# Kernel tuning notes

Hardware: AMD Instinct MI355X
Metric: run time of the kernel (lower is better)

The kernel has to match this reference:

```python
import jax, jax.numpy as jnp
import numpy as np

N_NODES = 50000
IN_DIM = 128
OUT_DIM = 128
HEADS = 4
HEAD_DIM = OUT_DIM // HEADS
N_EDGES = 800000
LN_EPS = 1e-5
NEG_SLOPE = 0.2


def setup_inputs() -> dict:
    key = jax.random.key(0)
    ks = jax.random.split(key, 8)
    x = jax.random.normal(ks[0], (N_NODES, IN_DIM), dtype=jnp.float32)
    edge_index = jax.random.randint(ks[1], (2, N_EDGES), 0, N_NODES, dtype=jnp.int64)
    s = 1.0 / np.sqrt(IN_DIM)
    W = jax.random.uniform(ks[2], (IN_DIM, HEADS * HEAD_DIM), jnp.float32, -s, s)
    att_src = jax.random.uniform(ks[3], (HEADS, HEAD_DIM), jnp.float32, -s, s)
    att_dst = jax.random.uniform(ks[4], (HEADS, HEAD_DIM), jnp.float32, -s, s)
    bias = jnp.zeros((OUT_DIM,), jnp.float32)
    gamma = jnp.ones((OUT_DIM,), jnp.float32)
    beta = jnp.zeros((OUT_DIM,), jnp.float32)
    return {"x": x, "edge_index": edge_index, "W": W, "att_src": att_src,
            "att_dst": att_dst, "bias": bias, "gamma": gamma, "beta": beta}


def reference(x, edge_index, W, att_src, att_dst, bias, gamma, beta):
    N = x.shape[0]
    H, C = att_src.shape
    # add self-loops (PyG GATConv default)
    loops = jnp.arange(N, dtype=edge_index.dtype)
    src = jnp.concatenate([edge_index[0], loops])  # [E+N]
    dst = jnp.concatenate([edge_index[1], loops])

    h = (x @ W).reshape(N, H, C)                      # [N,H,C]
    a_src = jnp.einsum('nhc,hc->nh', h, att_src)      # [N,H]
    a_dst = jnp.einsum('nhc,hc->nh', h, att_dst)

    e = jax.nn.leaky_relu(a_src[src] + a_dst[dst], NEG_SLOPE)   # [E+N,H]
    emax = jax.ops.segment_max(e, dst, num_segments=N)          # [N,H]
    ex = jnp.exp(e - emax[dst])
    denom = jax.ops.segment_sum(ex, dst, num_segments=N)
    alpha = ex / denom[dst]                                     # [E+N,H]

    msg = h[src] * alpha[:, :, None]                            # [E+N,H,C]
    out = jax.ops.segment_sum(msg, dst, num_segments=N).reshape(N, H * C) + bias

    # LayerNorm
    mu = out.mean(-1, keepdims=True)
    var = ((out - mu) ** 2).mean(-1, keepdims=True)
    hn = (out - mu) / jnp.sqrt(var + LN_EPS) * gamma + beta

    # residual is Identity (in_dim == out_dim); GELU exact; dropout = eval identity
    return jax.nn.gelu(hn + x, approximate=False)
```

## Files before the change

kernel.cpp:

```cpp
#include <hip/hip_runtime.h>
#include <math.h>

#define N_NODES 50000
#define HEADS 4
#define NEG_SLOPE 0.2f
#define LN_EPS 1e-5f
#define SLOTS 80
#define GR 64
#define EPB 2048
#define DSH 8
#define NB 196
#define CAP 40

typedef short short8 __attribute__((ext_vector_type(8)));
typedef float f32x4 __attribute__((ext_vector_type(4)));


__device__ __forceinline__ short f2bf(float f) {
    unsigned u = __float_as_uint(f);
    return (short)((u + 0x7fffu + ((u >> 16) & 1u)) >> 16);
}

__device__ __forceinline__ void load_edge(const int* __restrict__ ei, int e, int E,
                                          int is64, int& s, int& d) {
    if (is64) {
        s = ei[2 * e];
        d = ei[2 * (E + e)];
    } else {
        s = ei[e];
        d = ei[E + e];
    }
}

__device__ __forceinline__ int detect_is64(const int* __restrict__ ei, int t, int* s_flag) {
    if (t < 64) {
        int nz = (ei[2 * t + 1] != 0) ? 1 : 0;
        unsigned long long b = __ballot(nz);
        if (t == 0) *s_flag = (b == 0ULL) ? 1 : 0;
    }
    __syncthreads();
    return *s_flag;
}

__device__ __forceinline__ float s8f(unsigned u, int p) {
    return (float)((int)(u << (24 - 8 * p)) >> 24);
}

__device__ __forceinline__ float edge_w(float v) {
    v = v > 0.f ? v : NEG_SLOPE * v;
    return __expf(v);
}


__global__ __launch_bounds__(256, 4) void gemm_scatter_kernel(
    const float* __restrict__ x, const float* __restrict__ W,
    const float* __restrict__ att_src, const float* __restrict__ att_dst,
    unsigned* __restrict__ hb, float* __restrict__ hscale,
    float* __restrict__ a_src, float* __restrict__ a_dst,
    const int* __restrict__ ei, int E, int nScatter, int nGemm,
    unsigned* __restrict__ staging, int* __restrict__ scnt) {
    __shared__ __align__(16) char smem[40960];
    const int t = threadIdx.x;
    const int b = (int)blockIdx.x;

    const bool isBin = (b % 3) == 0;
    const int rid = isBin ? (b / 3) : (2 * (b / 3) + (b % 3) - 1);

    if (isBin) {
        if (rid >= nScatter) return;
        int is64 = detect_is64(ei, t, (int*)smem);
        int* lcnt = (int*)smem + 64;
        for (int i = t; i < NB; i += 256) lcnt[i] = 0;
        __syncthreads();

        const int e0 = rid * EPB + t;
        int ss[8], dd[8];
#pragma unroll
        for (int u = 0; u < 8; ++u) {
            int e = e0 + u * 256;
            if (e < E) {
                load_edge(ei, e, E, is64, ss[u], dd[u]);
            } else {
                ss[u] = -1; dd[u] = 0;
            }
        }
#pragma unroll
        for (int u = 0; u < 8; ++u) {
            if (ss[u] < 0) continue;
            int bkt = dd[u] >> DSH;
            int p = atomicAdd(&lcnt[bkt], 1);
            if (p < CAP)
                staging[((size_t)bkt * nScatter + rid) * CAP + p] =
                    (unsigned)ss[u] | ((unsigned)dd[u] << 16);
        }
        __syncthreads();
        for (int i = t; i < NB; i += 256)
            scnt[(size_t)i * nScatter + rid] = min(lcnt[i], CAP);
        return;
    }

    if (rid >= nGemm) return;
    const int rowBase = rid * GR;
    const int l = t & 63;
    const int wv = t >> 6;

    {
        const int nlo = l & 7, khi = l >> 3;
        for (int i = 0; i < 8; ++i) {
            int tile = wv + 4 * i;
            int n = (tile & 15) * 8 + nlo;
            int k8 = (tile >> 4) * 8 + khi;
            short8 pk;
#pragma unroll
            for (int jj = 0; jj < 8; ++jj)
                pk[jj] = f2bf(W[(k8 * 8 + jj) * 128 + n]);
            int us = (k8 & 8) | ((k8 & 7) ^ (n & 7));
            *(short8*)(smem + n * 256 + us * 16) = pk;
        }
    }
    __syncthreads();

    const int g = l >> 4;
    const int c = l & 15;

    f32x4 acc[8];
#pragma unroll
    for (int ct = 0; ct < 8; ++ct) acc[ct] = {0.f, 0.f, 0.f, 0.f};

    {
        int arow = rowBase + wv * 16 + c;
        if (arow >= N_NODES) arow = N_NODES - 1;
        const float* xrow = x + (size_t)arow * 128;
#pragma unroll
        for (int kk = 0; kk < 4; ++kk) {
            float4 xa = *(const float4*)(xrow + kk * 32 + g * 8);
            float4 xb = *(const float4*)(xrow + kk * 32 + g * 8 + 4);
            short8 af;
            af[0] = f2bf(xa.x); af[1] = f2bf(xa.y); af[2] = f2bf(xa.z); af[3] = f2bf(xa.w);
            af[4] = f2bf(xb.x); af[5] = f2bf(xb.y); af[6] = f2bf(xb.z); af[7] = f2bf(xb.w);
#pragma unroll
            for (int ct = 0; ct < 8; ++ct) {
                int n = ct * 16 + c;
                int u = kk * 4 + g;
                int us = (u & 8) | ((u & 7) ^ (n & 7));
                short8 bf = *(const short8*)(smem + n * 256 + us * 16);
                acc[ct] = __builtin_amdgcn_mfma_f32_16x16x32_bf16(af, bf, acc[ct], 0, 0, 0);
            }
        }
    }

    char* ep = smem + 32768 + wv * 2048;
    float asA[4], asB[4], adA[4], adB[4];
#pragma unroll
    for (int h = 0; h < 4; ++h) {
        asA[h] = att_src[h * 32 + c];
        asB[h] = att_src[h * 32 + 16 + c];
        adA[h] = att_dst[h * 32 + c];
        adB[h] = att_dst[h * 32 + 16 + c];
    }
#pragma unroll
    for (int r = 0; r < 4; ++r) {
        float v[8];
#pragma unroll
        for (int ct = 0; ct < 8; ++ct) v[ct] = acc[ct][r];

        float m = fabsf(v[0]);
#pragma unroll
        for (int ct = 1; ct < 8; ++ct) m = fmaxf(m, fabsf(v[ct]));
#pragma unroll
        for (int o = 1; o < 16; o <<= 1) m = fmaxf(m, __shfl_xor(m, o, 64));
        m = fmaxf(m, 1e-20f);
        const float inv = 127.0f / m;

        float sp[4], dp[4];
#pragma unroll
        for (int h = 0; h < 4; ++h) {
            sp[h] = v[2 * h] * asA[h] + v[2 * h + 1] * asB[h];
            dp[h] = v[2 * h] * adA[h] + v[2 * h + 1] * adB[h];
        }
#pragma unroll
        for (int o = 1; o < 16; o <<= 1) {
#pragma unroll
            for (int h = 0; h < 4; ++h) {
                sp[h] += __shfl_xor(sp[h], o, 64);
                dp[h] += __shfl_xor(dp[h], o, 64);
            }
        }
        const int row_l = g * 4 + r;
        const int row = rowBase + wv * 16 + row_l;
        if (c == 0 && row < N_NODES) {
            hscale[row] = m * (1.0f / 127.0f);
            a_src[row * 4 + 0] = sp[0]; a_src[row * 4 + 1] = sp[1];
            a_src[row * 4 + 2] = sp[2]; a_src[row * 4 + 3] = sp[3];
            a_dst[row * 4 + 0] = dp[0]; a_dst[row * 4 + 1] = dp[1];
            a_dst[row * 4 + 2] = dp[2]; a_dst[row * 4 + 3] = dp[3];
        }
#pragma unroll
        for (int ct = 0; ct < 8; ++ct) {
            int q = __float2int_rn(v[ct] * inv);
            ep[row_l * 128 + ct * 16 + c] = (char)q;
        }
    }

#pragma unroll
    for (int w8 = 0; w8 < 8; ++w8) {
        int idx = w8 * 64 + l;
        int row_l = idx >> 5, tx = idx & 31;
        unsigned word = *(const unsigned*)(ep + row_l * 128 + tx * 4);
        int row = rowBase + wv * 16 + row_l;
        if (row < N_NODES) hb[(size_t)row * 32 + tx] = word;
    }
}

__global__ __launch_bounds__(256) void build_kernel(
    const unsigned* __restrict__ staging, const int* __restrict__ scnt,
    int nScatter, int* __restrict__ cnt, unsigned short* __restrict__ esrc) {
    __shared__ int lcnt2[256];
    const int B = blockIdx.x;
    const int t = threadIdx.x;
    lcnt2[t] = 0;
    __syncthreads();

    for (int blk = t; blk < nScatter; blk += 256) {
        const int c = scnt[(size_t)B * nScatter + blk];
        const unsigned* cell = staging + ((size_t)B * nScatter + blk) * CAP;
        for (int j = 0; j < c; j += 4) {
            uint4 q = *(const uint4*)(cell + j);
            const int m = c - j;
            {
                int d = (int)(q.x >> 16);
                int p = atomicAdd(&lcnt2[d & 255], 1);
                if (p < SLOTS) esrc[(size_t)d * SLOTS + p] = (unsigned short)(q.x & 0xffffu);
            }
            if (m > 1) {
                int d = (int)(q.y >> 16);
                int p = atomicAdd(&lcnt2[d & 255], 1);
                if (p < SLOTS) esrc[(size_t)d * SLOTS + p] = (unsigned short)(q.y & 0xffffu);
            }
            if (m > 2) {
                int d = (int)(q.z >> 16);
                int p = atomicAdd(&lcnt2[d & 255], 1);
                if (p < SLOTS) esrc[(size_t)d * SLOTS + p] = (unsigned short)(q.z & 0xffffu);
            }
            if (m > 3) {
                int d = (int)(q.w >> 16);
                int p = atomicAdd(&lcnt2[d & 255], 1);
                if (p < SLOTS) esrc[(size_t)d * SLOTS + p] = (unsigned short)(q.w & 0xffffu);
            }
        }
    }
    __syncthreads();
    const int d = (B << DSH) + t;
    if (d < N_NODES) cnt[d] = lcnt2[t];
}

__global__ __launch_bounds__(256) void gat_fused_kernel(
    const int* __restrict__ cnt, const unsigned short* __restrict__ esrc,
    const float* __restrict__ a_src, const float* __restrict__ a_dst,
    const unsigned* __restrict__ hb, const float* __restrict__ hscale,
    const float* __restrict__ bias, const float* __restrict__ x,
    const float* __restrict__ gamma, const float* __restrict__ beta,
    float* __restrict__ out) {
    const int t = threadIdx.x;
    const int l = t & 63;
    const int wv = t >> 6;
    const int g = l >> 4;
    const int j = l & 15;
    const int n = blockIdx.x * 16 + wv * 4 + g;
    const int hh = j >> 2;

    const uint2* hb2 = (const uint2*)hb;

    const float adst_me = a_dst[(n << 2) + hh];
    float ps = edge_w(a_src[(n << 2) + hh] + adst_me);

    uint2 hvS = hb2[(unsigned)(n * 16 + j)];
    {
        const float uS = ps * hscale[n];
        float acc0 = uS * s8f(hvS.x, 0), acc1 = uS * s8f(hvS.x, 1);
        float acc2 = uS * s8f(hvS.x, 2), acc3 = uS * s8f(hvS.x, 3);
        float acc4 = uS * s8f(hvS.y, 0), acc5 = uS * s8f(hvS.y, 1);
        float acc6 = uS * s8f(hvS.y, 2), acc7 = uS * s8f(hvS.y, 3);

        const int deg = min(cnt[n], SLOTS);
        const unsigned short* row = esrc + n * SLOTS;

        for (int base = 0; base < deg; base += 8) {
            const int rem = deg - base;
            uint4 q = *(const uint4*)(row + base);
            int s0 = (int)(q.x & 0xffffu);
            int s1 = (rem > 1) ? (int)(q.x >> 16) : n;
            int s2 = (rem > 2) ? (int)(q.y & 0xffffu) : n;
            int s3 = (rem > 3) ? (int)(q.y >> 16) : n;
            int s4 = (rem > 4) ? (int)(q.z & 0xffffu) : n;
            int s5 = (rem > 5) ? (int)(q.z >> 16) : n;
            int s6 = (rem > 6) ? (int)(q.w & 0xffffu) : n;
            int s7 = (rem > 7) ? (int)(q.w >> 16) : n;

            float b0 = a_src[(s0 << 2) + hh];
            float b1 = a_src[(s1 << 2) + hh];
            float b2 = a_src[(s2 << 2) + hh];
            float b3 = a_src[(s3 << 2) + hh];
            float b4 = a_src[(s4 << 2) + hh];
            float b5 = a_src[(s5 << 2) + hh];
            float b6 = a_src[(s6 << 2) + hh];
            float b7 = a_src[(s7 << 2) + hh];
            float c0 = hscale[s0], c1 = hscale[s1], c2 = hscale[s2], c3 = hscale[s3];
            float c4 = hscale[s4], c5 = hscale[s5], c6 = hscale[s6], c7 = hscale[s7];
            uint2 h0 = hb2[(unsigned)(s0 * 16 + j)];
            uint2 h1 = hb2[(unsigned)(s1 * 16 + j)];
            uint2 h2 = hb2[(unsigned)(s2 * 16 + j)];
            uint2 h3 = hb2[(unsigned)(s3 * 16 + j)];
            uint2 h4 = hb2[(unsigned)(s4 * 16 + j)];
            uint2 h5 = hb2[(unsigned)(s5 * 16 + j)];
            uint2 h6 = hb2[(unsigned)(s6 * 16 + j)];
            uint2 h7 = hb2[(unsigned)(s7 * 16 + j)];

            float w0 = edge_w(b0 + adst_me);
            float w1 = (rem > 1) ? edge_w(b1 + adst_me) : 0.f;
            float w2 = (rem > 2) ? edge_w(b2 + adst_me) : 0.f;
            float w3 = (rem > 3) ? edge_w(b3 + adst_me) : 0.f;
            float w4 = (rem > 4) ? edge_w(b4 + adst_me) : 0.f;
            float w5 = (rem > 5) ? edge_w(b5 + adst_me) : 0.f;
            float w6 = (rem > 6) ? edge_w(b6 + adst_me) : 0.f;
            float w7 = (rem > 7) ? edge_w(b7 + adst_me) : 0.f;
            ps += (w0 + w1 + w2 + w3) + (w4 + w5 + w6 + w7);

            float u0 = w0 * c0, u1 = w1 * c1, u2 = w2 * c2, u3 = w3 * c3;
            float u4 = w4 * c4, u5 = w5 * c5, u6 = w6 * c6, u7 = w7 * c7;

            acc0 += u0 * s8f(h0.x, 0) + u1 * s8f(h1.x, 0) + u2 * s8f(h2.x, 0) + u3 * s8f(h3.x, 0)
                  + u4 * s8f(h4.x, 0) + u5 * s8f(h5.x, 0) + u6 * s8f(h6.x, 0) + u7 * s8f(h7.x, 0);
            acc1 += u0 * s8f(h0.x, 1) + u1 * s8f(h1.x, 1) + u2 * s8f(h2.x, 1) + u3 * s8f(h3.x, 1)
                  + u4 * s8f(h4.x, 1) + u5 * s8f(h5.x, 1) + u6 * s8f(h6.x, 1) + u7 * s8f(h7.x, 1);
            acc2 += u0 * s8f(h0.x, 2) + u1 * s8f(h1.x, 2) + u2 * s8f(h2.x, 2) + u3 * s8f(h3.x, 2)
                  + u4 * s8f(h4.x, 2) + u5 * s8f(h5.x, 2) + u6 * s8f(h6.x, 2) + u7 * s8f(h7.x, 2);
            acc3 += u0 * s8f(h0.x, 3) + u1 * s8f(h1.x, 3) + u2 * s8f(h2.x, 3) + u3 * s8f(h3.x, 3)
                  + u4 * s8f(h4.x, 3) + u5 * s8f(h5.x, 3) + u6 * s8f(h6.x, 3) + u7 * s8f(h7.x, 3);
            acc4 += u0 * s8f(h0.y, 0) + u1 * s8f(h1.y, 0) + u2 * s8f(h2.y, 0) + u3 * s8f(h3.y, 0)
                  + u4 * s8f(h4.y, 0) + u5 * s8f(h5.y, 0) + u6 * s8f(h6.y, 0) + u7 * s8f(h7.y, 0);
            acc5 += u0 * s8f(h0.y, 1) + u1 * s8f(h1.y, 1) + u2 * s8f(h2.y, 1) + u3 * s8f(h3.y, 1)
                  + u4 * s8f(h4.y, 1) + u5 * s8f(h5.y, 1) + u6 * s8f(h6.y, 1) + u7 * s8f(h7.y, 1);
            acc6 += u0 * s8f(h0.y, 2) + u1 * s8f(h1.y, 2) + u2 * s8f(h2.y, 2) + u3 * s8f(h3.y, 2)
                  + u4 * s8f(h4.y, 2) + u5 * s8f(h5.y, 2) + u6 * s8f(h6.y, 2) + u7 * s8f(h7.y, 2);
            acc7 += u0 * s8f(h0.y, 3) + u1 * s8f(h1.y, 3) + u2 * s8f(h2.y, 3) + u3 * s8f(h3.y, 3)
                  + u4 * s8f(h4.y, 3) + u5 * s8f(h5.y, 3) + u6 * s8f(h6.y, 3) + u7 * s8f(h7.y, 3);
        }

        const float inv = 1.0f / ps;
        const float4* bias4 = (const float4*)bias;
        float4 bA = bias4[j * 2], bB = bias4[j * 2 + 1];
        float v0 = acc0 * inv + bA.x, v1 = acc1 * inv + bA.y;
        float v2 = acc2 * inv + bA.z, v3 = acc3 * inv + bA.w;
        float v4 = acc4 * inv + bB.x, v5 = acc5 * inv + bB.y;
        float v6 = acc6 * inv + bB.z, v7 = acc7 * inv + bB.w;

        float s1 = v0 + v1 + v2 + v3 + v4 + v5 + v6 + v7;
        float s2 = v0 * v0 + v1 * v1 + v2 * v2 + v3 * v3 +
                   v4 * v4 + v5 * v5 + v6 * v6 + v7 * v7;
#pragma unroll
        for (int o = 1; o < 16; o <<= 1) {
            s1 += __shfl_xor(s1, o, 64);
            s2 += __shfl_xor(s2, o, 64);
        }
        float mu = s1 * (1.0f / 128.0f);
        float var = s2 * (1.0f / 128.0f) - mu * mu;
        float rstd = rsqrtf(var + LN_EPS);

        const float4* gamma4 = (const float4*)gamma;
        const float4* beta4 = (const float4*)beta;
        const float4* x4 = (const float4*)x;
        float4 gA = gamma4[j * 2], gB = gamma4[j * 2 + 1];
        float4 eA = beta4[j * 2], eB = beta4[j * 2 + 1];
        float4 xA = x4[(size_t)n * 32 + j * 2], xB = x4[(size_t)n * 32 + j * 2 + 1];

        float r0 = (v0 - mu) * rstd * gA.x + eA.x + xA.x;
        float r1 = (v1 - mu) * rstd * gA.y + eA.y + xA.y;
        float r2 = (v2 - mu) * rstd * gA.z + eA.z + xA.z;
        float r3 = (v3 - mu) * rstd * gA.w + eA.w + xA.w;
        float r4 = (v4 - mu) * rstd * gB.x + eB.x + xB.x;
        float r5 = (v5 - mu) * rstd * gB.y + eB.y + xB.y;
        float r6 = (v6 - mu) * rstd * gB.z + eB.z + xB.z;
        float r7 = (v7 - mu) * rstd * gB.w + eB.w + xB.w;

        const float k = 0.70710678118654752440f;
        float4 oA = make_float4(0.5f * r0 * (1.0f + erff(r0 * k)),
                                0.5f * r1 * (1.0f + erff(r1 * k)),
                                0.5f * r2 * (1.0f + erff(r2 * k)),
                                0.5f * r3 * (1.0f + erff(r3 * k)));
        float4 oB = make_float4(0.5f * r4 * (1.0f + erff(r4 * k)),
                                0.5f * r5 * (1.0f + erff(r5 * k)),
                                0.5f * r6 * (1.0f + erff(r6 * k)),
                                0.5f * r7 * (1.0f + erff(r7 * k)));
        float4* out4 = (float4*)out;
        out4[(size_t)n * 32 + j * 2] = oA;
        out4[(size_t)n * 32 + j * 2 + 1] = oB;
    }
}


extern "C" void kernel_launch(void* const* d_in, const int* in_sizes, int n_in,
                              void* d_out, int out_size, void* d_ws, size_t ws_size,
                              hipStream_t stream) {
    const float* x       = (const float*)d_in[0];
    const int*   ei      = (const int*)d_in[1];
    const float* W       = (const float*)d_in[2];
    const float* att_src = (const float*)d_in[3];
    const float* att_dst = (const float*)d_in[4];
    const float* bias    = (const float*)d_in[5];
    const float* gamma   = (const float*)d_in[6];
    const float* beta    = (const float*)d_in[7];
    float* out = (float*)d_out;
    const int E = in_sizes[1] / 2;

    unsigned* hb         = (unsigned*)d_ws;
    float* hscale        = (float*)(hb + (size_t)N_NODES * 32);
    float* a_src         = hscale + N_NODES;
    float* a_dst         = a_src + N_NODES * 4;
    int*   cnt           = (int*)(a_dst + N_NODES * 4);
    unsigned short* esrc = (unsigned short*)(cnt + N_NODES);

    const int nScatter = (E + EPB - 1) / EPB;
    unsigned* staging    = (unsigned*)(esrc + (size_t)N_NODES * SLOTS);
    int* scnt            = (int*)(staging + (size_t)NB * nScatter * CAP);

    const int nGemm = (N_NODES + GR - 1) / GR;
    int total = 3 * nScatter;
    const int needGemm = 3 * ((nGemm + 1) / 2);
    if (needGemm > total) total = needGemm;

    gemm_scatter_kernel<<<total, 256, 0, stream>>>(
        x, W, att_src, att_dst, hb, hscale, a_src, a_dst, ei, E, nScatter, nGemm,
        staging, scnt);
    build_kernel<<<NB, 256, 0, stream>>>(staging, scnt, nScatter, cnt, esrc);
    gat_fused_kernel<<<N_NODES / 16, 256, 0, stream>>>(cnt, esrc, a_src, a_dst, hb,
                                                       hscale, bias, x, gamma, beta, out);
}
```

Measured before the change: 147.3 us.

## Pack per-node a_src and scale into the quantized feature row; vectorize edge loads

```diff
diff --git a/kernel.cpp b/kernel.cpp
--- a/kernel.cpp
+++ b/kernel.cpp
@@ -11,6 +11,7 @@
 #define DSH 8
 #define NB 196
 #define CAP 40
+#define HBW 40
 
 typedef short short8 __attribute__((ext_vector_type(8)));
 typedef float f32x4 __attribute__((ext_vector_type(4)));
@@ -19,17 +20,6 @@
 __device__ __forceinline__ short f2bf(float f) {
     unsigned u = __float_as_uint(f);
     return (short)((u + 0x7fffu + ((u >> 16) & 1u)) >> 16);
-}
-
-__device__ __forceinline__ void load_edge(const int* __restrict__ ei, int e, int E,
-                                          int is64, int& s, int& d) {
-    if (is64) {
-        s = ei[2 * e];
-        d = ei[2 * (E + e)];
-    } else {
-        s = ei[e];
-        d = ei[E + e];
-    }
 }
 
 __device__ __forceinline__ int detect_is64(const int* __restrict__ ei, int t, int* s_flag) {
@@ -55,8 +45,7 @@
 __global__ __launch_bounds__(256, 4) void gemm_scatter_kernel(
     const float* __restrict__ x, const float* __restrict__ W,
     const float* __restrict__ att_src, const float* __restrict__ att_dst,
-    unsigned* __restrict__ hb, float* __restrict__ hscale,
-    float* __restrict__ a_src, float* __restrict__ a_dst,
+    unsigned* __restrict__ hb, float* __restrict__ a_dst,
     const int* __restrict__ ei, int E, int nScatter, int nGemm,
     unsigned* __restrict__ staging, int* __restrict__ scnt) {
     __shared__ __align__(16) char smem[40960];
@@ -73,15 +62,38 @@
         for (int i = t; i < NB; i += 256) lcnt[i] = 0;
         __syncthreads();
 
-        const int e0 = rid * EPB + t;
+        const int e0 = rid * EPB + t * 8;
         int ss[8], dd[8];
-#pragma unroll
-        for (int u = 0; u < 8; ++u) {
-            int e = e0 + u * 256;
-            if (e < E) {
-                load_edge(ei, e, E, is64, ss[u], dd[u]);
+        if (e0 + 8 <= E) {
+            if (is64) {
+                const uint4* ps4 = (const uint4*)(ei + 2 * (size_t)e0);
+                const uint4* pd4 = (const uint4*)(ei + 2 * ((size_t)E + e0));
+#pragma unroll
+                for (int u = 0; u < 4; ++u) {
+                    uint4 qs = ps4[u], qd = pd4[u];
+                    ss[2 * u] = (int)qs.x; ss[2 * u + 1] = (int)qs.z;
+                    dd[2 * u] = (int)qd.x; dd[2 * u + 1] = (int)qd.z;
+                }
             } else {
-                ss[u] = -1; dd[u] = 0;
+                const uint4* ps4 = (const uint4*)(ei + e0);
+                const uint4* pd4 = (const uint4*)(ei + (size_t)E + e0);
+#pragma unroll
+                for (int u = 0; u < 2; ++u) {
+                    uint4 qs = ps4[u], qd = pd4[u];
+                    ss[4 * u] = (int)qs.x; ss[4 * u + 1] = (int)qs.y;
+                    ss[4 * u + 2] = (int)qs.z; ss[4 * u + 3] = (int)qs.w;
+                    dd[4 * u] = (int)qd.x; dd[4 * u + 1] = (int)qd.y;
+                    dd[4 * u + 2] = (int)qd.z; dd[4 * u + 3] = (int)qd.w;
+                }
+            }
+        } else {
+#pragma unroll
+            for (int u = 0; u < 8; ++u) {
+                int e = e0 + u;
+                if (e < E) {
+                    if (is64) { ss[u] = ei[2 * e]; dd[u] = ei[2 * (E + e)]; }
+                    else      { ss[u] = ei[e];     dd[u] = ei[E + e]; }
+                } else { ss[u] = -1; dd[u] = 0; }
             }
         }
 #pragma unroll
@@ -189,9 +201,10 @@
         const int row_l = g * 4 + r;
         const int row = rowBase + wv * 16 + row_l;
         if (c == 0 && row < N_NODES) {
-            hscale[row] = m * (1.0f / 127.0f);
-            a_src[row * 4 + 0] = sp[0]; a_src[row * 4 + 1] = sp[1];
-            a_src[row * 4 + 2] = sp[2]; a_src[row * 4 + 3] = sp[3];
+            const float hs = m * (1.0f / 127.0f);
+            float4* rw = (float4*)(hb + (size_t)row * HBW + 32);
+            rw[0] = make_float4(sp[0], hs, sp[1], hs);
+            rw[1] = make_float4(sp[2], hs, sp[3], hs);
             a_dst[row * 4 + 0] = dp[0]; a_dst[row * 4 + 1] = dp[1];
             a_dst[row * 4 + 2] = dp[2]; a_dst[row * 4 + 3] = dp[3];
         }
@@ -208,7 +221,7 @@
         int row_l = idx >> 5, tx = idx & 31;
         unsigned word = *(const unsigned*)(ep + row_l * 128 + tx * 4);
         int row = rowBase + wv * 16 + row_l;
-        if (row < N_NODES) hb[(size_t)row * 32 + tx] = word;
+        if (row < N_NODES) hb[(size_t)row * HBW + tx] = word;
     }
 }
 
@@ -256,8 +269,8 @@
 
 __global__ __launch_bounds__(256) void gat_fused_kernel(
     const int* __restrict__ cnt, const unsigned short* __restrict__ esrc,
-    const float* __restrict__ a_src, const float* __restrict__ a_dst,
-    const unsigned* __restrict__ hb, const float* __restrict__ hscale,
+    const float* __restrict__ a_dst,
+    const unsigned* __restrict__ hb,
     const float* __restrict__ bias, const float* __restrict__ x,
     const float* __restrict__ gamma, const float* __restrict__ beta,
     float* __restrict__ out) {
@@ -272,11 +285,12 @@
     const uint2* hb2 = (const uint2*)hb;
 
     const float adst_me = a_dst[(n << 2) + hh];
-    float ps = edge_w(a_src[(n << 2) + hh] + adst_me);
-
-    uint2 hvS = hb2[(unsigned)(n * 16 + j)];
+    uint2 rS = hb2[(unsigned)(n * 20 + 16 + hh)];
+    float ps = edge_w(__uint_as_float(rS.x) + adst_me);
+
+    uint2 hvS = hb2[(unsigned)(n * 20 + j)];
     {
-        const float uS = ps * hscale[n];
+        const float uS = ps * __uint_as_float(rS.y);
         float acc0 = uS * s8f(hvS.x, 0), acc1 = uS * s8f(hvS.x, 1);
         float acc2 = uS * s8f(hvS.x, 2), acc3 = uS * s8f(hvS.x, 3);
         float acc4 = uS * s8f(hvS.y, 0), acc5 = uS * s8f(hvS.y, 1);
@@ -297,37 +311,37 @@
             int s6 = (rem > 6) ? (int)(q.w & 0xffffu) : n;
             int s7 = (rem > 7) ? (int)(q.w >> 16) : n;
 
-            float b0 = a_src[(s0 << 2) + hh];
-            float b1 = a_src[(s1 << 2) + hh];
-            float b2 = a_src[(s2 << 2) + hh];
-            float b3 = a_src[(s3 << 2) + hh];
-            float b4 = a_src[(s4 << 2) + hh];
-            float b5 = a_src[(s5 << 2) + hh];
-            float b6 = a_src[(s6 << 2) + hh];
-            float b7 = a_src[(s7 << 2) + hh];
-            float c0 = hscale[s0], c1 = hscale[s1], c2 = hscale[s2], c3 = hscale[s3];
-            float c4 = hscale[s4], c5 = hscale[s5], c6 = hscale[s6], c7 = hscale[s7];
-            uint2 h0 = hb2[(unsigned)(s0 * 16 + j)];
-            uint2 h1 = hb2[(unsigned)(s1 * 16 + j)];
-            uint2 h2 = hb2[(unsigned)(s2 * 16 + j)];
-            uint2 h3 = hb2[(unsigned)(s3 * 16 + j)];
-            uint2 h4 = hb2[(unsigned)(s4 * 16 + j)];
-            uint2 h5 = hb2[(unsigned)(s5 * 16 + j)];
-            uint2 h6 = hb2[(unsigned)(s6 * 16 + j)];
-            uint2 h7 = hb2[(unsigned)(s7 * 16 + j)];
-
-            float w0 = edge_w(b0 + adst_me);
-            float w1 = (rem > 1) ? edge_w(b1 + adst_me) : 0.f;
-            float w2 = (rem > 2) ? edge_w(b2 + adst_me) : 0.f;
-            float w3 = (rem > 3) ? edge_w(b3 + adst_me) : 0.f;
-            float w4 = (rem > 4) ? edge_w(b4 + adst_me) : 0.f;
-            float w5 = (rem > 5) ? edge_w(b5 + adst_me) : 0.f;
-            float w6 = (rem > 6) ? edge_w(b6 + adst_me) : 0.f;
-            float w7 = (rem > 7) ? edge_w(b7 + adst_me) : 0.f;
+            uint2 r0 = hb2[(unsigned)(s0 * 20 + 16 + hh)];
+            uint2 r1 = hb2[(unsigned)(s1 * 20 + 16 + hh)];
+            uint2 r2 = hb2[(unsigned)(s2 * 20 + 16 + hh)];
+            uint2 r3 = hb2[(unsigned)(s3 * 20 + 16 + hh)];
+            uint2 r4 = hb2[(unsigned)(s4 * 20 + 16 + hh)];
+            uint2 r5 = hb2[(unsigned)(s5 * 20 + 16 + hh)];
+            uint2 r6 = hb2[(unsigned)(s6 * 20 + 16 + hh)];
+            uint2 r7 = hb2[(unsigned)(s7 * 20 + 16 + hh)];
+            uint2 h0 = hb2[(unsigned)(s0 * 20 + j)];
+            uint2 h1 = hb2[(unsigned)(s1 * 20 + j)];
+            uint2 h2 = hb2[(unsigned)(s2 * 20 + j)];
+            uint2 h3 = hb2[(unsigned)(s3 * 20 + j)];
+            uint2 h4 = hb2[(unsigned)(s4 * 20 + j)];
+            uint2 h5 = hb2[(unsigned)(s5 * 20 + j)];
+            uint2 h6 = hb2[(unsigned)(s6 * 20 + j)];
+            uint2 h7 = hb2[(unsigned)(s7 * 20 + j)];
+
+            float w0 = edge_w(__uint_as_float(r0.x) + adst_me);
+            float w1 = (rem > 1) ? edge_w(__uint_as_float(r1.x) + adst_me) : 0.f;
+            float w2 = (rem > 2) ? edge_w(__uint_as_float(r2.x) + adst_me) : 0.f;
+            float w3 = (rem > 3) ? edge_w(__uint_as_float(r3.x) + adst_me) : 0.f;
+            float w4 = (rem > 4) ? edge_w(__uint_as_float(r4.x) + adst_me) : 0.f;
+            float w5 = (rem > 5) ? edge_w(__uint_as_float(r5.x) + adst_me) : 0.f;
+            float w6 = (rem > 6) ? edge_w(__uint_as_float(r6.x) + adst_me) : 0.f;
+            float w7 = (rem > 7) ? edge_w(__uint_as_float(r7.x) + adst_me) : 0.f;
             ps += (w0 + w1 + w2 + w3) + (w4 + w5 + w6 + w7);
 
-            float u0 = w0 * c0, u1 = w1 * c1, u2 = w2 * c2, u3 = w3 * c3;
-            float u4 = w4 * c4, u5 = w5 * c5, u6 = w6 * c6, u7 = w7 * c7;
+            float u0 = w0 * __uint_as_float(r0.y), u1 = w1 * __uint_as_float(r1.y);
+            float u2 = w2 * __uint_as_float(r2.y), u3 = w3 * __uint_as_float(r3.y);
+            float u4 = w4 * __uint_as_float(r4.y), u5 = w5 * __uint_as_float(r5.y);
+            float u6 = w6 * __uint_as_float(r6.y), u7 = w7 * __uint_as_float(r7.y);
 
             acc0 += u0 * s8f(h0.x, 0) + u1 * s8f(h1.x, 0) + u2 * s8f(h2.x, 0) + u3 * s8f(h3.x, 0)
                   + u4 * s8f(h4.x, 0) + u5 * s8f(h5.x, 0) + u6 * s8f(h6.x, 0) + u7 * s8f(h7.x, 0);
@@ -374,24 +388,24 @@
         float4 eA = beta4[j * 2], eB = beta4[j * 2 + 1];
         float4 xA = x4[(size_t)n * 32 + j * 2], xB = x4[(size_t)n * 32 + j * 2 + 1];
 
-        float r0 = (v0 - mu) * rstd * gA.x + eA.x + xA.x;
-        float r1 = (v1 - mu) * rstd * gA.y + eA.y + xA.y;
-        float r2 = (v2 - mu) * rstd * gA.z + eA.z + xA.z;
-        float r3 = (v3 - mu) * rstd * gA.w + eA.w + xA.w;
-        float r4 = (v4 - mu) * rstd * gB.x + eB.x + xB.x;
-        float r5 = (v5 - mu) * rstd * gB.y + eB.y + xB.y;
-        float r6 = (v6 - mu) * rstd * gB.z + eB.z + xB.z;
-        float r7 = (v7 - mu) * rstd * gB.w + eB.w + xB.w;
+        float r0f = (v0 - mu) * rstd * gA.x + eA.x + xA.x;
+        float r1f = (v1 - mu) * rstd * gA.y + eA.y + xA.y;
+        float r2f = (v2 - mu) * rstd * gA.z + eA.z + xA.z;
+        float r3f = (v3 - mu) * rstd * gA.w + eA.w + xA.w;
+        float r4f = (v4 - mu) * rstd * gB.x + eB.x + xB.x;
+        float r5f = (v5 - mu) * rstd * gB.y + eB.y + xB.y;
+        float r6f = (v6 - mu) * rstd * gB.z + eB.z + xB.z;
+        float r7f = (v7 - mu) * rstd * gB.w + eB.w + xB.w;
 
         const float k = 0.70710678118654752440f;
-        float4 oA = make_float4(0.5f * r0 * (1.0f + erff(r0 * k)),
-                                0.5f * r1 * (1.0f + erff(r1 * k)),
-                                0.5f * r2 * (1.0f + erff(r2 * k)),
-                                0.5f * r3 * (1.0f + erff(r3 * k)));
-        float4 oB = make_float4(0.5f * r4 * (1.0f + erff(r4 * k)),
-                                0.5f * r5 * (1.0f + erff(r5 * k)),
-                                0.5f * r6 * (1.0f + erff(r6 * k)),
-                                0.5f * r7 * (1.0f + erff(r7 * k)));
+        float4 oA = make_float4(0.5f * r0f * (1.0f + erff(r0f * k)),
+                                0.5f * r1f * (1.0f + erff(r1f * k)),
+                                0.5f * r2f * (1.0f + erff(r2f * k)),
+                                0.5f * r3f * (1.0f + erff(r3f * k)));
+        float4 oB = make_float4(0.5f * r4f * (1.0f + erff(r4f * k)),
+                                0.5f * r5f * (1.0f + erff(r5f * k)),
+                                0.5f * r6f * (1.0f + erff(r6f * k)),
+                                0.5f * r7f * (1.0f + erff(r7f * k)));
         float4* out4 = (float4*)out;
         out4[(size_t)n * 32 + j * 2] = oA;
         out4[(size_t)n * 32 + j * 2 + 1] = oB;
@@ -414,9 +428,7 @@
     const int E = in_sizes[1] / 2;
 
     unsigned* hb         = (unsigned*)d_ws;
-    float* hscale        = (float*)(hb + (size_t)N_NODES * 32);
-    float* a_src         = hscale + N_NODES;
-    float* a_dst         = a_src + N_NODES * 4;
+    float* a_dst         = (float*)(hb + (size_t)N_NODES * HBW);
     int*   cnt           = (int*)(a_dst + N_NODES * 4);
     unsigned short* esrc = (unsigned short*)(cnt + N_NODES);
 
@@ -430,9 +442,9 @@
     if (needGemm > total) total = needGemm;
 
     gemm_scatter_kernel<<<total, 256, 0, stream>>>(
-        x, W, att_src, att_dst, hb, hscale, a_src, a_dst, ei, E, nScatter, nGemm,
+        x, W, att_src, att_dst, hb, a_dst, ei, E, nScatter, nGemm,
         staging, scnt);
     build_kernel<<<NB, 256, 0, stream>>>(staging, scnt, nScatter, cnt, esrc);
-    gat_fused_kernel<<<N_NODES / 16, 256, 0, stream>>>(cnt, esrc, a_src, a_dst, hb,
-                                                       hscale, bias, x, gamma, beta, out);
-}
+    gat_fused_kernel<<<N_NODES / 16, 256, 0, stream>>>(cnt, esrc, a_dst, hb,
+                                                       bias, x, gamma, beta, out);
+}
```

After: 150.9 us. 2.4% more time.
